# Optimization experiments

Measured on AMD Instinct MI355X. Metric: run time of the kernel, lower is better.

Reference implementation:

```python
import jax, jax.numpy as jnp
import numpy as np

L, H, C, V, BLK = 6, 16, 1024, 32000, 2048
B, T, TA = 2, 512, 512
DFF = 4 * C
STD = 0.02
PROJ_STD = 0.02 / np.sqrt(2 * L)  # c_proj init per module
SCALE = 1.0 / np.sqrt(C // H)


def setup_inputs() -> dict:
    key = jax.random.key(0)
    ks = iter(jax.random.split(key, 64))
    nrm = lambda shape, std=STD: jax.random.normal(next(ks), shape, jnp.float32) * std
    inp = {
        'idx': jax.random.randint(next(ks), (B, T), 0, V),
        'xa': jax.random.normal(next(ks), (B, TA, C), jnp.float32),
        'wte': nrm((V, C)),            # tied with lm_head
        'wpe': nrm((BLK, C)),
        'ln1_w': jnp.ones((L, C)), 'ln1_b': jnp.zeros((L, C)),
        'sa_wq': nrm((L, C, C)), 'sa_bq': jnp.zeros((L, C)),
        'sa_wk': nrm((L, C, C)), 'sa_bk': jnp.zeros((L, C)),
        'sa_wv': nrm((L, C, C)), 'sa_bv': jnp.zeros((L, C)),
        'sa_wo': nrm((L, C, C), PROJ_STD), 'sa_bo': jnp.zeros((L, C)),
        'ca_wq': nrm((L, C, C)), 'ca_bq': jnp.zeros((L, C)),
        'ca_wk': nrm((L, C, C)), 'ca_bk': jnp.zeros((L, C)),
        'ca_wv': nrm((L, C, C)), 'ca_bv': jnp.zeros((L, C)),
        'ca_wo': nrm((L, C, C), PROJ_STD), 'ca_bo': jnp.zeros((L, C)),
        'ln2_w': jnp.ones((L, C)), 'ln2_b': jnp.zeros((L, C)),
        'fc_w': nrm((L, C, DFF)), 'fc_b': jnp.zeros((L, DFF)),
        'pr_w': nrm((L, DFF, C), PROJ_STD), 'pr_b': jnp.zeros((L, C)),
        'lnf_w': jnp.ones((C,)), 'lnf_b': jnp.zeros((C,)),
    }
    return inp


def _ln(h, w, b):
    m = h.mean(-1, keepdims=True)
    v = jnp.mean((h - m) ** 2, -1, keepdims=True)
    return (h - m) * jax.lax.rsqrt(v + 1e-5) * w + b


def _gelu(h):  # new_gelu (tanh approximation)
    return 0.5 * h * (1.0 + jnp.tanh(np.sqrt(2.0 / np.pi) * (h + 0.044715 * h ** 3)))


def _attn(hq, hkv, wq, bq, wk, bk, wv, bv, wo, bo):
    # NB: the original applies a tril causal mask even for cross-attention.
    Bq, Tq, _ = hq.shape
    Tk = hkv.shape[1]
    D = C // H
    q = (hq @ wq + bq).reshape(Bq, Tq, H, D)
    k = (hkv @ wk + bk).reshape(Bq, Tk, H, D)
    v = (hkv @ wv + bv).reshape(Bq, Tk, H, D)
    att = jnp.einsum('bqhd,bkhd->bhqk', q, k) * SCALE
    mask = jnp.tril(jnp.ones((Tq, Tk), bool))
    att = jnp.where(mask, att, -jnp.inf)
    att = jax.nn.softmax(att, axis=-1)
    y = jnp.einsum('bhqk,bkhd->bqhd', att, v).reshape(Bq, Tq, C)
    return y @ wo + bo


def _forward(idx, xa, wte, wpe, ln1_w, ln1_b, sa_wq, sa_bq, sa_wk, sa_bk, sa_wv, sa_bv, sa_wo, sa_bo,
             ca_wq, ca_bq, ca_wk, ca_bk, ca_wv, ca_bv, ca_wo, ca_bo,
             ln2_w, ln2_b, fc_w, fc_b, pr_w, pr_b, lnf_w, lnf_b):
    t = idx.shape[1]
    x = wte[idx] + wpe[:t][None]  # [B,T,C]

    def block(h, p):
        (l1w, l1b, sqw, sqb, skw, skb, svw, svb, sow, sob,
         cqw, cqb, ckw, ckb, cvw, cvb, cow, cob,
         l2w, l2b, fw, fb, pw, pb) = p
        n = _ln(h, l1w, l1b)
        h = h + _attn(n, n, sqw, sqb, skw, skb, svw, svb, sow, sob)
        n = _ln(h, l1w, l1b)  # ln_1 reused for cross-attn, as in source
        h = h + _attn(n, xa, cqw, cqb, ckw, ckb, cvw, cvb, cow, cob)
        n = _ln(h, l2w, l2b)
        h = h + (_gelu(n @ fw + fb) @ pw + pb)
        return h, None

    xs = (ln1_w, ln1_b, sa_wq, sa_bq, sa_wk, sa_bk, sa_wv, sa_bv, sa_wo, sa_bo,
          ca_wq, ca_bq, ca_wk, ca_bk, ca_wv, ca_bv, ca_wo, ca_bo,
          ln2_w, ln2_b, fc_w, fc_b, pr_w, pr_b)
    x, _ = jax.lax.scan(block, x, xs)
    x = _ln(x, lnf_w, lnf_b)
    return x @ wte.T  # tied lm_head, [B,T,V]


def reference(idx, xa, wte, wpe, ln1_w, ln1_b, sa_wq, sa_bq, sa_wk, sa_bk, sa_wv, sa_bv, sa_wo, sa_bo,
              ca_wq, ca_bq, ca_wk, ca_bk, ca_wv, ca_bv, ca_wo, ca_bo,
              ln2_w, ln2_b, fc_w, fc_b, pr_w, pr_b, lnf_w, lnf_b):
    return _forward(idx, xa, wte, wpe, ln1_w, ln1_b, sa_wq, sa_bq, sa_wk, sa_bk, sa_wv, sa_bv, sa_wo, sa_bo,
                    ca_wq, ca_bq, ca_wk, ca_bk, ca_wv, ca_bv, ca_wo, ca_bo,
                    ln2_w, ln2_b, fc_w, fc_b, pr_w, pr_b, lnf_w, lnf_b)
```

## Files before the change

kernel.cpp:

```cpp
#include <hip/hip_runtime.h>
#include <math.h>

#define CC   1024
#define HH   16
#define DH   64
#define TT   512
#define NTOK 1024
#define DFF_ 4096
#define VV   32000
#define QKSCALE 0.125f

typedef unsigned short u16;
typedef __attribute__((ext_vector_type(8))) short short8;
typedef __attribute__((ext_vector_type(4))) float f32x4;

__device__ __forceinline__ u16 f2bf(float f) {
  union { float f; unsigned u; } v; v.f = f;
  unsigned r = v.u + 0x7FFFu + ((v.u >> 16) & 1u);
  return (u16)(r >> 16);
}
__device__ __forceinline__ float gelu_f(float h) {
  return 0.5f * h * (1.0f + tanhf(0.7978845608028654f * (h + 0.044715f * h * h * h)));
}

#define GLD16(gp, lp) __builtin_amdgcn_global_load_lds( \
    (const __attribute__((address_space(1))) void*)(gp), \
    (__attribute__((address_space(3))) void*)(lp), 16, 0, 0)

#define MFMA(a, b, c) __builtin_amdgcn_mfma_f32_16x16x32_bf16(a, b, c, 0, 0, 0)

__global__ __launch_bounds__(256) void embed_kernel(
    const int* __restrict__ idx, const float* __restrict__ wte,
    const float* __restrict__ wpe, float* __restrict__ x) {
  int row = blockIdx.x;
  int t = row & (TT - 1);
  int id = idx[row];
  const float4* a = (const float4*)(wte + (size_t)id * CC);
  const float4* p = (const float4*)(wpe + (size_t)t * CC);
  float4* o = (float4*)(x + (size_t)row * CC);
  int c = threadIdx.x;
  float4 va = a[c], vp = p[c];
  float4 ov;
  ov.x = va.x + vp.x; ov.y = va.y + vp.y; ov.z = va.z + vp.z; ov.w = va.w + vp.w;
  o[c] = ov;
}

__global__ __launch_bounds__(256) void ln_kernel(
    const float* __restrict__ x, const float* __restrict__ w,
    const float* __restrict__ b, u16* __restrict__ out) {
  int row = blockIdx.x, tid = threadIdx.x;
  float4 v = ((const float4*)(x + (size_t)row * CC))[tid];
  float s  = v.x + v.y + v.z + v.w;
  float sq = fmaf(v.x, v.x, fmaf(v.y, v.y, fmaf(v.z, v.z, v.w * v.w)));
  for (int o = 32; o > 0; o >>= 1) { s += __shfl_down(s, o); sq += __shfl_down(sq, o); }
  __shared__ float rs[4], rq[4];
  int wid = tid >> 6, lane = tid & 63;
  if (lane == 0) { rs[wid] = s; rq[wid] = sq; }
  __syncthreads();
  s  = rs[0] + rs[1] + rs[2] + rs[3];
  sq = rq[0] + rq[1] + rq[2] + rq[3];
  float mean = s * (1.0f / CC);
  float var  = sq * (1.0f / CC) - mean * mean;
  float rstd = 1.0f / sqrtf(var + 1e-5f);
  float4 wv = ((const float4*)w)[tid];
  float4 bv = ((const float4*)b)[tid];
  ushort4 o;
  o.x = f2bf((v.x - mean) * rstd * wv.x + bv.x);
  o.y = f2bf((v.y - mean) * rstd * wv.y + bv.y);
  o.z = f2bf((v.z - mean) * rstd * wv.z + bv.z);
  o.w = f2bf((v.w - mean) * rstd * wv.w + bv.w);
  ((ushort4*)(out + (size_t)row * CC))[tid] = o;
}

__global__ __launch_bounds__(256) void wtrans16_kernel(
    const float* __restrict__ w0, const float* __restrict__ w1,
    const float* __restrict__ w2, const float* __restrict__ w3,
    const float* __restrict__ w4, const float* __restrict__ w5,
    const float* __restrict__ w6, const float* __restrict__ w7,
    const float* __restrict__ fc, const float* __restrict__ pr,
    u16* __restrict__ wt) {
  const size_t M1 = 1048576;
  int z = blockIdx.z;
  const float* src;
  size_t doff;
  int sstr, dstr;
  if (z < 8) {
    src = z == 0 ? w0 : z == 1 ? w1 : z == 2 ? w2 : z == 3 ? w3
        : z == 4 ? w4 : z == 5 ? w5 : z == 6 ? w6 : w7;
    sstr = 1024; doff = (size_t)z * M1; dstr = 1024;
  } else if (z < 12) {
    int s = z - 8;
    src = fc + (size_t)s * 1024; sstr = 4096;
    doff = 8 * M1 + (size_t)s * M1; dstr = 1024;
  } else {
    int s = z - 12;
    src = pr + (size_t)s * M1; sstr = 1024;
    doff = 12 * M1 + (size_t)s * 1024; dstr = 4096;
  }
  __shared__ float t[32][33];
  int bx = blockIdx.x * 32, by = blockIdx.y * 32;
  int c = threadIdx.x & 31, r = threadIdx.x >> 5;
#pragma unroll
  for (int i = 0; i < 4; ++i)
    t[r + i * 8][c] = src[(size_t)(by + r + i * 8) * sstr + bx + c];
  __syncthreads();
#pragma unroll
  for (int i = 0; i < 4; ++i)
    wt[doff + (size_t)(bx + r + i * 8) * dstr + by + c] = f2bf(t[c][r + i * 8]);
}

__global__ __launch_bounds__(256) void convbf_kernel(
    const float* __restrict__ in, u16* __restrict__ out, int n4) {
  int i = blockIdx.x * 256 + threadIdx.x;
  if (i < n4) {
    float4 v = ((const float4*)in)[i];
    ushort4 o; o.x = f2bf(v.x); o.y = f2bf(v.y); o.z = f2bf(v.z); o.w = f2bf(v.w);
    ((ushort4*)out)[i] = o;
  }
}

template <int EPI, int MODE, int BM, int BN, int BK>
__global__ __launch_bounds__(256) void gemm_bf16_kernel(
    const u16* __restrict__ A, const u16* __restrict__ B,
    const float* __restrict__ bias, const float* __restrict__ bias2,
    const float* __restrict__ bias3, float* __restrict__ Cm,
    int K, int ldc, int whichbase) {
  constexpr int WM = BM / 2, WN = BN / 2, MF = WM / 16, NF = WN / 16;
  constexpr int KS = BK / 32;
  constexpr int NB = BK / 8;
  constexpr int PA = BM * BK / 2048;
  constexpr int PB = BN * BK / 2048;
  constexpr int RPP = 2048 / BK;
  __shared__ u16 As[2][BM * BK];
  __shared__ u16 Bs[2][BN * BK];
  int tid = threadIdx.x;
  int lane = tid & 63, wave = tid >> 6;
  int wr = wave >> 1, wc = wave & 1;
  int row0, col0;
  if (MODE == 2) {
    int id = blockIdx.x;
    int wg = (id & 7) * 250 + (id >> 3);
    row0 = (wg & 7) * BM;
    col0 = (wg >> 3) * BN;
  } else {
    row0 = blockIdx.y * BM;
    col0 = blockIdx.x * BN;
  }
  f32x4 acc[MF][NF];
#pragma unroll
  for (int m = 0; m < MF; ++m)
#pragma unroll
    for (int n = 0; n < NF; ++n) acc[m][n] = (f32x4){0.f, 0.f, 0.f, 0.f};

  int srow = tid / NB;
  int sblk = (BK == 64) ? ((tid & 7) ^ ((tid >> 3) & 7))
                        : ((tid & 3) ^ ((tid >> 3) & 3));
  const u16* Ab = A + (size_t)row0 * K;
  const u16* Bb = B + (size_t)col0 * K;
  int arow = wr * WM + (lane & 15);
  int brow = wc * WN + (lane & 15);
  int g8 = lane >> 4;

  auto stage = [&](int bufi, int k0) {
#pragma unroll
    for (int p = 0; p < PA; ++p)
      GLD16(Ab + (size_t)(p * RPP + srow) * K + k0 + sblk * 8,
            &As[bufi][p * 2048 + wave * 512]);
#pragma unroll
    for (int p = 0; p < PB; ++p)
      GLD16(Bb + (size_t)(p * RPP + srow) * K + k0 + sblk * 8,
            &Bs[bufi][p * 2048 + wave * 512]);
  };

  const int NT = K / BK;
  stage(0, 0);
  __syncthreads();
  for (int t = 0; t < NT; ++t) {
    int cur = t & 1;
    if (t + 1 < NT) stage(cur ^ 1, (t + 1) * BK);
    const u16* Ac = As[cur];
    const u16* Bc = Bs[cur];
#pragma unroll
    for (int ks = 0; ks < KS; ++ks) {
      short8 af[MF], bg[NF];
#pragma unroll
      for (int m = 0; m < MF; ++m) {
        int row = arow + m * 16;
        int off = (BK == 64) ? row * 64 + (((ks * 4 + g8) ^ (row & 7)) << 3)
                             : row * 32 + ((g8 ^ ((row >> 1) & 3)) << 3);
        af[m] = *(const short8*)&Ac[off];
      }
#pragma unroll
      for (int n = 0; n < NF; ++n) {
        int row = brow + n * 16;
        int off = (BK == 64) ? row * 64 + (((ks * 4 + g8) ^ (row & 7)) << 3)
                             : row * 32 + ((g8 ^ ((row >> 1) & 3)) << 3);
        bg[n] = *(const short8*)&Bc[off];
      }
      __builtin_amdgcn_s_setprio(1);
#pragma unroll
      for (int m = 0; m < MF; ++m)
#pragma unroll
        for (int n = 0; n < NF; ++n)
          acc[m][n] = MFMA(af[m], bg[n], acc[m][n]);
      __builtin_amdgcn_s_setprio(0);
    }
    __syncthreads();
  }

  int r0 = row0 + wr * WM + g8 * 4;
  int c0 = col0 + wc * WN + (lane & 15);

  if (EPI == 4) {
    u16* qb = (u16*)Cm;
#pragma unroll
    for (int m = 0; m < MF; ++m)
#pragma unroll
      for (int n = 0; n < NF; ++n) {
        int j = c0 + n * 16;
        int which = whichbase + (j >> 10);
        const float* bp = (j >> 10) == 0 ? bias : ((j >> 10) == 1 ? bias2 : bias3);
        float bj = bp ? bp[j & 1023] : 0.0f;
        int h = (j & 1023) >> 6, d = j & 63;
        int trow0 = r0 + m * 16;
        int b = trow0 >> 9, t0 = trow0 & 511;
        int bh = b * 16 + h;
        u16 vals[4];
#pragma unroll
        for (int r = 0; r < 4; ++r) vals[r] = f2bf(acc[m][n][r] + bj);
        if (which < 2) {
          u16* dst = qb + (size_t)which * 1048576 + (size_t)bh * 32768 + (size_t)t0 * 64 + d;
#pragma unroll
          for (int r = 0; r < 4; ++r) dst[(size_t)r * 64] = vals[r];
        } else {
          u16* dst = qb + 2 * 1048576 + (size_t)bh * 32768 + (size_t)d * 512 + t0;
          *(ushort4*)dst = *(ushort4*)vals;
        }
      }
    return;
  }

  float bj[NF];
#pragma unroll
  for (int n = 0; n < NF; ++n)
    bj[n] = bias ? bias[c0 + n * 16] : 0.0f;
  u16* Cb = (u16*)Cm;
#pragma unroll
  for (int m = 0; m < MF; ++m)
#pragma unroll
    for (int n = 0; n < NF; ++n)
#pragma unroll
      for (int r = 0; r < 4; ++r) {
        size_t off = (size_t)(r0 + m * 16 + r) * ldc + c0 + n * 16;
        float v = acc[m][n][r] + bj[n];
        if (EPI == 0) Cm[off] = v;
        else if (EPI == 1) Cm[off] += v;
        else if (EPI == 2) Cb[off] = f2bf(gelu_f(v));
      }
}

__global__ __launch_bounds__(256) void attn_kernel(
    const u16* __restrict__ qh, const u16* __restrict__ kh,
    const u16* __restrict__ vt, u16* __restrict__ y) {
  __shared__ u16 P[32 * 512];
  __shared__ float smax[4][32], ssum[4][32];
  int tid = threadIdx.x, lane = tid & 63, w = tid >> 6;
  int bx = blockIdx.x, bh = blockIdx.y;
  int q0 = bx * 32;
  int b = bh >> 4, h = bh & 15;
  const u16* qb = qh + (size_t)bh * 32768;
  const u16* kb = kh + (size_t)bh * 32768;
  const u16* vb = vt + (size_t)bh * 32768;
  int g = lane >> 4, c = lane & 15;

  short8 a[2][2];
#pragma unroll
  for (int rt = 0; rt < 2; ++rt)
#pragma unroll
    for (int ks = 0; ks < 2; ++ks)
      a[rt][ks] = *(const short8*)(qb + (size_t)(q0 + rt * 16 + c) * 64 + ks * 32 + g * 8);

  int lim = q0 + 31;
  int nct = (lim - w * 128) / 16 + 1;
  if (nct > 8) nct = 8;
  if (nct < 0) nct = 0;
  f32x4 s[2][8];
#pragma unroll
  for (int rt = 0; rt < 2; ++rt)
#pragma unroll
    for (int ct = 0; ct < 8; ++ct) s[rt][ct] = (f32x4){0.f, 0.f, 0.f, 0.f};
  for (int ct = 0; ct < nct; ++ct) {
    int n0 = w * 128 + ct * 16;
#pragma unroll
    for (int ks = 0; ks < 2; ++ks) {
      short8 bf = *(const short8*)(kb + (size_t)(n0 + c) * 64 + ks * 32 + g * 8);
      s[0][ct] = MFMA(a[0][ks], bf, s[0][ct]);
      s[1][ct] = MFMA(a[1][ks], bf, s[1][ct]);
    }
  }

  float mx[2][4];
#pragma unroll
  for (int rt = 0; rt < 2; ++rt)
#pragma unroll
    for (int r = 0; r < 4; ++r) mx[rt][r] = -1e30f;
  for (int ct = 0; ct < nct; ++ct) {
    int col = w * 128 + ct * 16 + c;
#pragma unroll
    for (int rt = 0; rt < 2; ++rt)
#pragma unroll
      for (int r = 0; r < 4; ++r) {
        int trow = q0 + rt * 16 + g * 4 + r;
        float v = s[rt][ct][r] * QKSCALE;
        if (col > trow) v = -1e30f;
        s[rt][ct][r] = v;
        mx[rt][r] = fmaxf(mx[rt][r], v);
      }
  }
#pragma unroll
  for (int off = 1; off < 16; off <<= 1)
#pragma unroll
    for (int rt = 0; rt < 2; ++rt)
#pragma unroll
      for (int r = 0; r < 4; ++r) mx[rt][r] = fmaxf(mx[rt][r], __shfl_xor(mx[rt][r], off));
  if (c == 0)
#pragma unroll
    for (int rt = 0; rt < 2; ++rt)
#pragma unroll
      for (int r = 0; r < 4; ++r) smax[w][rt * 16 + g * 4 + r] = mx[rt][r];
  __syncthreads();

  float m_[2][4], sum[2][4];
#pragma unroll
  for (int rt = 0; rt < 2; ++rt)
#pragma unroll
    for (int r = 0; r < 4; ++r) {
      int row = rt * 16 + g * 4 + r;
      m_[rt][r] = fmaxf(fmaxf(smax[0][row], smax[1][row]), fmaxf(smax[2][row], smax[3][row]));
      sum[rt][r] = 0.f;
    }
  for (int ct = 0; ct < nct; ++ct) {
    int col = w * 128 + ct * 16 + c;
    int blk = col >> 3, cl = col & 7;
#pragma unroll
    for (int rt = 0; rt < 2; ++rt)
#pragma unroll
      for (int r = 0; r < 4; ++r) {
        float p = __expf(s[rt][ct][r] - m_[rt][r]);
        sum[rt][r] += p;
        int row = rt * 16 + g * 4 + r;
        int hsh = (row ^ (row >> 2)) & 7;
        P[row * 512 + ((blk ^ hsh) << 3) + cl] = f2bf(p);
      }
  }
#pragma unroll
  for (int off = 1; off < 16; off <<= 1)
#pragma unroll
    for (int rt = 0; rt < 2; ++rt)
#pragma unroll
      for (int r = 0; r < 4; ++r) sum[rt][r] += __shfl_xor(sum[rt][r], off);
  if (c == 0)
#pragma unroll
    for (int rt = 0; rt < 2; ++rt)
#pragma unroll
      for (int r = 0; r < 4; ++r) ssum[w][rt * 16 + g * 4 + r] = sum[rt][r];
  __syncthreads();

  float li[2][4];
#pragma unroll
  for (int rt = 0; rt < 2; ++rt)
#pragma unroll
    for (int r = 0; r < 4; ++r) {
      int row = rt * 16 + g * 4 + r;
      li[rt][r] = 1.0f / (ssum[0][row] + ssum[1][row] + ssum[2][row] + ssum[3][row]);
    }

  int rt2 = w >> 1, nh = w & 1;
  f32x4 o[2];
  o[0] = (f32x4){0.f, 0.f, 0.f, 0.f};
  o[1] = (f32x4){0.f, 0.f, 0.f, 0.f};
  int nks = bx + 1;
  int prow = rt2 * 16 + c;
  int phsh = (prow ^ (prow >> 2)) & 7;
  for (int ks = 0; ks < nks; ++ks) {
    short8 pa = *(const short8*)&P[prow * 512 + (((ks * 4 + g) ^ phsh) << 3)];
#pragma unroll
    for (int nt = 0; nt < 2; ++nt) {
      int d = nh * 32 + nt * 16 + c;
      short8 vf = *(const short8*)(vb + (size_t)d * 512 + ks * 32 + g * 8);
      o[nt] = MFMA(pa, vf, o[nt]);
    }
  }
#pragma unroll
  for (int nt = 0; nt < 2; ++nt)
#pragma unroll
    for (int r = 0; r < 4; ++r) {
      int trow = q0 + rt2 * 16 + g * 4 + r;
      float val = o[nt][r] * li[rt2][r];
      y[(size_t)(b * 512 + trow) * 1024 + h * 64 + nh * 32 + nt * 16 + c] = f2bf(val);
    }
}

extern "C" void kernel_launch(void* const* d_in, const int* in_sizes, int n_in,
                              void* d_out, int out_size, void* d_ws, size_t ws_size,
                              hipStream_t stream) {
  const int*   idx   = (const int*)d_in[0];
  const float* xa    = (const float*)d_in[1];
  const float* wte   = (const float*)d_in[2];
  const float* wpe   = (const float*)d_in[3];
  const float* ln1_w = (const float*)d_in[4];
  const float* ln1_b = (const float*)d_in[5];
  const float* sa_wq = (const float*)d_in[6];
  const float* sa_bq = (const float*)d_in[7];
  const float* sa_wk = (const float*)d_in[8];
  const float* sa_bk = (const float*)d_in[9];
  const float* sa_wv = (const float*)d_in[10];
  const float* sa_bv = (const float*)d_in[11];
  const float* sa_wo = (const float*)d_in[12];
  const float* sa_bo = (const float*)d_in[13];
  const float* ca_wq = (const float*)d_in[14];
  const float* ca_bq = (const float*)d_in[15];
  const float* ca_wk = (const float*)d_in[16];
  const float* ca_bk = (const float*)d_in[17];
  const float* ca_wv = (const float*)d_in[18];
  const float* ca_bv = (const float*)d_in[19];
  const float* ca_wo = (const float*)d_in[20];
  const float* ca_bo = (const float*)d_in[21];
  const float* ln2_w = (const float*)d_in[22];
  const float* ln2_b = (const float*)d_in[23];
  const float* fc_w  = (const float*)d_in[24];
  const float* fc_b  = (const float*)d_in[25];
  const float* pr_w  = (const float*)d_in[26];
  const float* pr_b  = (const float*)d_in[27];
  const float* lnf_w = (const float*)d_in[28];
  const float* lnf_b = (const float*)d_in[29];

  const size_t M1 = 1048576;
  float* ws     = (float*)d_ws;
  float* x      = ws;
  u16* qkvh  = (u16*)(x + M1);
  u16* nbf   = qkvh + 3 * M1;
  u16* ybf   = nbf + M1;
  u16* hmbf  = ybf + M1;
  u16* xabf  = hmbf + 4 * M1;
  u16* wtebf = xabf + M1;
  u16* wT    = wtebf + (size_t)VV * CC;

  const size_t oQKV = 0, oWO = 3 * M1, oCQ = 4 * M1, oCKV = 5 * M1,
               oCWO = 7 * M1, oFC = 8 * M1, oPR = 12 * M1;

  embed_kernel<<<NTOK, 256, 0, stream>>>(idx, wte, wpe, x);
  convbf_kernel<<<(VV * CC / 4 + 255) / 256, 256, 0, stream>>>(wte, wtebf, VV * CC / 4);
  convbf_kernel<<<(NTOK * CC / 4 + 255) / 256, 256, 0, stream>>>(xa, xabf, NTOK * CC / 4);

  for (int l = 0; l < 6; ++l) {
    size_t wofs = (size_t)l * CC * CC;
    size_t bofs = (size_t)l * CC;
    size_t mofs = (size_t)l * CC * DFF_;

    wtrans16_kernel<<<dim3(32, 32, 16), 256, 0, stream>>>(
        sa_wq + wofs, sa_wk + wofs, sa_wv + wofs, sa_wo + wofs,
        ca_wq + wofs, ca_wk + wofs, ca_wv + wofs, ca_wo + wofs,
        fc_w + mofs, pr_w + mofs, wT);

    ln_kernel<<<NTOK, 256, 0, stream>>>(x, ln1_w + bofs, ln1_b + bofs, nbf);
    gemm_bf16_kernel<4, 0, 64, 128, 64><<<dim3(24, 16), 256, 0, stream>>>(
        nbf, wT + oQKV, sa_bq + bofs, sa_bk + bofs, sa_bv + bofs,
        (float*)qkvh, CC, 0, 0);
    attn_kernel<<<dim3(16, 32), 256, 0, stream>>>(qkvh, qkvh + M1, qkvh + 2 * M1, ybf);
    gemm_bf16_kernel<1, 0, 64, 64, 64><<<dim3(16, 16), 256, 0, stream>>>(
        ybf, wT + oWO, sa_bo + bofs, nullptr, nullptr, x, CC, CC, 0);

    ln_kernel<<<NTOK, 256, 0, stream>>>(x, ln1_w + bofs, ln1_b + bofs, nbf);
    gemm_bf16_kernel<4, 0, 64, 64, 64><<<dim3(16, 16), 256, 0, stream>>>(
        nbf, wT + oCQ, ca_bq + bofs, nullptr, nullptr, (float*)qkvh, CC, 0, 0);
    gemm_bf16_kernel<4, 0, 64, 128, 64><<<dim3(16, 16), 256, 0, stream>>>(
        xabf, wT + oCKV, ca_bk + bofs, ca_bv + bofs, nullptr,
        (float*)qkvh, CC, 0, 1);
    attn_kernel<<<dim3(16, 32), 256, 0, stream>>>(qkvh, qkvh + M1, qkvh + 2 * M1, ybf);
    gemm_bf16_kernel<1, 0, 64, 64, 64><<<dim3(16, 16), 256, 0, stream>>>(
        ybf, wT + oCWO, ca_bo + bofs, nullptr, nullptr, x, CC, CC, 0);

    ln_kernel<<<NTOK, 256, 0, stream>>>(x, ln2_w + bofs, ln2_b + bofs, nbf);
    gemm_bf16_kernel<2, 0, 128, 128, 32><<<dim3(32, 8), 256, 0, stream>>>(
        nbf, wT + oFC, fc_b + (size_t)l * DFF_, nullptr, nullptr,
        (float*)hmbf, CC, DFF_, 0);
    gemm_bf16_kernel<1, 0, 64, 64, 64><<<dim3(16, 16), 256, 0, stream>>>(
        hmbf, wT + oPR, pr_b + bofs, nullptr, nullptr, x, DFF_, CC, 0);
  }

  ln_kernel<<<NTOK, 256, 0, stream>>>(x, lnf_w, lnf_b, nbf);
  gemm_bf16_kernel<0, 2, 128, 128, 32><<<dim3(2000), 256, 0, stream>>>(
      nbf, wtebf, nullptr, nullptr, nullptr, (float*)d_out, CC, VV, 0);
}
```

Measured before the change: 1.670 ms.

## Fuse wte bf16 conversion into lm_head GEMM, batch weight transposes, merge cross-attn QKV

The lm_head GEMM now reads fp32 wte directly and converts it to bf16 in registers while staging into LDS. This removes the separate full-vocab conversion pass and its 64MB bf16 copy. All six layers' weight transposes run in one launch when the workspace is large enough, and cross-attention Q and KV projections are merged into a single MODE-3 launch. Several GEMM tile shapes are also changed (smaller BM for the output projections, BK=64 for FC). The lm_head B load is now synchronous register staging instead of async global-to-LDS, which may expose more latency.

```diff
diff --git a/kernel.cpp b/kernel.cpp
--- a/kernel.cpp
+++ b/kernel.cpp
@@ -72,30 +72,34 @@
   ((ushort4*)(out + (size_t)row * CC))[tid] = o;
 }
 
-__global__ __launch_bounds__(256) void wtrans16_kernel(
+__global__ __launch_bounds__(256) void wtransL_kernel(
     const float* __restrict__ w0, const float* __restrict__ w1,
     const float* __restrict__ w2, const float* __restrict__ w3,
     const float* __restrict__ w4, const float* __restrict__ w5,
     const float* __restrict__ w6, const float* __restrict__ w7,
     const float* __restrict__ fc, const float* __restrict__ pr,
-    u16* __restrict__ wt) {
+    u16* __restrict__ wt, size_t dls, int lbase) {
   const size_t M1 = 1048576;
   int z = blockIdx.z;
+  int l = lbase + (z >> 4), slot = z & 15;
+  size_t wofs = (size_t)l * M1;
+  size_t mofs = (size_t)l * 4 * M1;
   const float* src;
-  size_t doff;
+  size_t doff = (size_t)(l - lbase) * dls;
   int sstr, dstr;
-  if (z < 8) {
-    src = z == 0 ? w0 : z == 1 ? w1 : z == 2 ? w2 : z == 3 ? w3
-        : z == 4 ? w4 : z == 5 ? w5 : z == 6 ? w6 : w7;
-    sstr = 1024; doff = (size_t)z * M1; dstr = 1024;
-  } else if (z < 12) {
-    int s = z - 8;
-    src = fc + (size_t)s * 1024; sstr = 4096;
-    doff = 8 * M1 + (size_t)s * M1; dstr = 1024;
+  if (slot < 8) {
+    const float* base = slot == 0 ? w0 : slot == 1 ? w1 : slot == 2 ? w2
+                      : slot == 3 ? w3 : slot == 4 ? w4 : slot == 5 ? w5
+                      : slot == 6 ? w6 : w7;
+    src = base + wofs; sstr = 1024; doff += (size_t)slot * M1; dstr = 1024;
+  } else if (slot < 12) {
+    int s = slot - 8;
+    src = fc + mofs + (size_t)s * 1024; sstr = 4096;
+    doff += 8 * M1 + (size_t)s * M1; dstr = 1024;
   } else {
-    int s = z - 12;
-    src = pr + (size_t)s * M1; sstr = 1024;
-    doff = 12 * M1 + (size_t)s * 1024; dstr = 4096;
+    int s = slot - 12;
+    src = pr + mofs + (size_t)s * M1; sstr = 1024;
+    doff += 12 * M1 + (size_t)s * 1024; dstr = 4096;
   }
   __shared__ float t[32][33];
   int bx = blockIdx.x * 32, by = blockIdx.y * 32;
@@ -121,7 +125,8 @@
 
 template <int EPI, int MODE, int BM, int BN, int BK>
 __global__ __launch_bounds__(256) void gemm_bf16_kernel(
-    const u16* __restrict__ A, const u16* __restrict__ B,
+    const u16* __restrict__ A, const u16* __restrict__ A2,
+    const u16* __restrict__ B, const u16* __restrict__ B2,
     const float* __restrict__ bias, const float* __restrict__ bias2,
     const float* __restrict__ bias3, float* __restrict__ Cm,
     int K, int ldc, int whichbase) {
@@ -137,11 +142,21 @@
   int lane = tid & 63, wave = tid >> 6;
   int wr = wave >> 1, wc = wave & 1;
   int row0, col0;
+  bool isq = true;
+  const u16* Ause = A;
+  const u16* Buse = B;
   if (MODE == 2) {
     int id = blockIdx.x;
     int wg = (id & 7) * 250 + (id >> 3);
     row0 = (wg & 7) * BM;
     col0 = (wg >> 3) * BN;
+  } else if (MODE == 3) {
+    int bx = blockIdx.x;
+    isq = bx < (1024 / BN);
+    Ause = isq ? A : A2;
+    Buse = isq ? B : B2;
+    col0 = (isq ? bx : bx - 1024 / BN) * BN;
+    row0 = blockIdx.y * BM;
   } else {
     row0 = blockIdx.y * BM;
     col0 = blockIdx.x * BN;
@@ -155,31 +170,13 @@
   int srow = tid / NB;
   int sblk = (BK == 64) ? ((tid & 7) ^ ((tid >> 3) & 7))
                         : ((tid & 3) ^ ((tid >> 3) & 3));
-  const u16* Ab = A + (size_t)row0 * K;
-  const u16* Bb = B + (size_t)col0 * K;
+  const u16* Ab = Ause + (size_t)row0 * K;
   int arow = wr * WM + (lane & 15);
   int brow = wc * WN + (lane & 15);
   int g8 = lane >> 4;
-
-  auto stage = [&](int bufi, int k0) {
-#pragma unroll
-    for (int p = 0; p < PA; ++p)
-      GLD16(Ab + (size_t)(p * RPP + srow) * K + k0 + sblk * 8,
-            &As[bufi][p * 2048 + wave * 512]);
-#pragma unroll
-    for (int p = 0; p < PB; ++p)
-      GLD16(Bb + (size_t)(p * RPP + srow) * K + k0 + sblk * 8,
-            &Bs[bufi][p * 2048 + wave * 512]);
-  };
-
   const int NT = K / BK;
-  stage(0, 0);
-  __syncthreads();
-  for (int t = 0; t < NT; ++t) {
-    int cur = t & 1;
-    if (t + 1 < NT) stage(cur ^ 1, (t + 1) * BK);
-    const u16* Ac = As[cur];
-    const u16* Bc = Bs[cur];
+
+  auto compute = [&](const u16* Ac, const u16* Bc) {
 #pragma unroll
     for (int ks = 0; ks < KS; ++ks) {
       short8 af[MF], bg[NF];
@@ -205,7 +202,65 @@
           acc[m][n] = MFMA(af[m], bg[n], acc[m][n]);
       __builtin_amdgcn_s_setprio(0);
     }
+  };
+
+  if constexpr (MODE == 2) {
+    const float* Bf = (const float*)B;
+    int bsr = tid >> 2;
+    int bkb = tid & 3;
+    float4 rb0, rb1, rb2, rb3;
+    auto loadB = [&](int k0) {
+      const float* p0 = Bf + (size_t)(col0 + bsr) * 1024 + k0 + bkb * 8;
+      const float* p1 = Bf + (size_t)(col0 + 64 + bsr) * 1024 + k0 + bkb * 8;
+      rb0 = *(const float4*)p0; rb1 = *(const float4*)(p0 + 4);
+      rb2 = *(const float4*)p1; rb3 = *(const float4*)(p1 + 4);
+    };
+    auto writeB = [&](int bufi) {
+      u16 t0[8] = {f2bf(rb0.x), f2bf(rb0.y), f2bf(rb0.z), f2bf(rb0.w),
+                   f2bf(rb1.x), f2bf(rb1.y), f2bf(rb1.z), f2bf(rb1.w)};
+      u16 t1[8] = {f2bf(rb2.x), f2bf(rb2.y), f2bf(rb2.z), f2bf(rb2.w),
+                   f2bf(rb3.x), f2bf(rb3.y), f2bf(rb3.z), f2bf(rb3.w)};
+      int r1 = 64 + bsr;
+      *(short8*)&Bs[bufi][bsr * 32 + ((bkb ^ ((bsr >> 1) & 3)) << 3)] = *(short8*)t0;
+      *(short8*)&Bs[bufi][r1 * 32 + ((bkb ^ ((r1 >> 1) & 3)) << 3)] = *(short8*)t1;
+    };
+    auto stageA = [&](int bufi, int k0) {
+#pragma unroll
+      for (int p = 0; p < PA; ++p)
+        GLD16(Ab + (size_t)(p * RPP + srow) * K + k0 + sblk * 8,
+              &As[bufi][p * 2048 + wave * 512]);
+    };
+    loadB(0);
+    stageA(0, 0);
+    writeB(0);
     __syncthreads();
+    for (int t = 0; t < NT; ++t) {
+      int cur = t & 1;
+      if (t + 1 < NT) { loadB((t + 1) * BK); stageA(cur ^ 1, (t + 1) * BK); }
+      compute(As[cur], Bs[cur]);
+      if (t + 1 < NT) writeB(cur ^ 1);
+      __syncthreads();
+    }
+  } else {
+    const u16* Bb = Buse + (size_t)col0 * K;
+    auto stage = [&](int bufi, int k0) {
+#pragma unroll
+      for (int p = 0; p < PA; ++p)
+        GLD16(Ab + (size_t)(p * RPP + srow) * K + k0 + sblk * 8,
+              &As[bufi][p * 2048 + wave * 512]);
+#pragma unroll
+      for (int p = 0; p < PB; ++p)
+        GLD16(Bb + (size_t)(p * RPP + srow) * K + k0 + sblk * 8,
+              &Bs[bufi][p * 2048 + wave * 512]);
+    };
+    stage(0, 0);
+    __syncthreads();
+    for (int t = 0; t < NT; ++t) {
+      int cur = t & 1;
+      if (t + 1 < NT) stage(cur ^ 1, (t + 1) * BK);
+      compute(As[cur], Bs[cur]);
+      __syncthreads();
+    }
   }
 
   int r0 = row0 + wr * WM + g8 * 4;
@@ -218,8 +273,8 @@
 #pragma unroll
       for (int n = 0; n < NF; ++n) {
         int j = c0 + n * 16;
-        int which = whichbase + (j >> 10);
-        const float* bp = (j >> 10) == 0 ? bias : ((j >> 10) == 1 ? bias2 : bias3);
+        int which = (MODE == 3 ? (isq ? 0 : 1) : whichbase) + (j >> 10);
+        const float* bp = which == 0 ? bias : (which == 1 ? bias2 : bias3);
         float bj = bp ? bp[j & 1023] : 0.0f;
         int h = (j & 1023) >> 6, d = j & 63;
         int trow0 = r0 + m * 16;
@@ -443,53 +498,59 @@
   u16* ybf   = nbf + M1;
   u16* hmbf  = ybf + M1;
   u16* xabf  = hmbf + 4 * M1;
-  u16* wtebf = xabf + M1;
-  u16* wT    = wtebf + (size_t)VV * CC;
+  u16* wT    = xabf + M1;
+
+  const bool full = ws_size >= 226492416ull;
+  const size_t wls = full ? 16 * M1 : 0;
 
   const size_t oQKV = 0, oWO = 3 * M1, oCQ = 4 * M1, oCKV = 5 * M1,
                oCWO = 7 * M1, oFC = 8 * M1, oPR = 12 * M1;
 
   embed_kernel<<<NTOK, 256, 0, stream>>>(idx, wte, wpe, x);
-  convbf_kernel<<<(VV * CC / 4 + 255) / 256, 256, 0, stream>>>(wte, wtebf, VV * CC / 4);
   convbf_kernel<<<(NTOK * CC / 4 + 255) / 256, 256, 0, stream>>>(xa, xabf, NTOK * CC / 4);
+  if (full)
+    wtransL_kernel<<<dim3(32, 32, 96), 256, 0, stream>>>(
+        sa_wq, sa_wk, sa_wv, sa_wo, ca_wq, ca_wk, ca_wv, ca_wo,
+        fc_w, pr_w, wT, wls, 0);
 
   for (int l = 0; l < 6; ++l) {
-    size_t wofs = (size_t)l * CC * CC;
     size_t bofs = (size_t)l * CC;
-    size_t mofs = (size_t)l * CC * DFF_;
-
-    wtrans16_kernel<<<dim3(32, 32, 16), 256, 0, stream>>>(
-        sa_wq + wofs, sa_wk + wofs, sa_wv + wofs, sa_wo + wofs,
-        ca_wq + wofs, ca_wk + wofs, ca_wv + wofs, ca_wo + wofs,
-        fc_w + mofs, pr_w + mofs, wT);
+    u16* wTl = wT + (size_t)l * wls;
+
+    if (!full)
+      wtransL_kernel<<<dim3(32, 32, 16), 256, 0, stream>>>(
+          sa_wq, sa_wk, sa_wv, sa_wo, ca_wq, ca_wk, ca_wv, ca_wo,
+          fc_w, pr_w, wT, 0, l);
 
     ln_kernel<<<NTOK, 256, 0, stream>>>(x, ln1_w + bofs, ln1_b + bofs, nbf);
     gemm_bf16_kernel<4, 0, 64, 128, 64><<<dim3(24, 16), 256, 0, stream>>>(
-        nbf, wT + oQKV, sa_bq + bofs, sa_bk + bofs, sa_bv + bofs,
-        (float*)qkvh, CC, 0, 0);
+        nbf, nullptr, wTl + oQKV, nullptr, sa_bq + bofs, sa_bk + bofs,
+        sa_bv + bofs, (float*)qkvh, CC, 0, 0);
     attn_kernel<<<dim3(16, 32), 256, 0, stream>>>(qkvh, qkvh + M1, qkvh + 2 * M1, ybf);
-    gemm_bf16_kernel<1, 0, 64, 64, 64><<<dim3(16, 16), 256, 0, stream>>>(
-        ybf, wT + oWO, sa_bo + bofs, nullptr, nullptr, x, CC, CC, 0);
+    gemm_bf16_kernel<1, 0, 32, 64, 64><<<dim3(16, 32), 256, 0, stream>>>(
+        ybf, nullptr, wTl + oWO, nullptr, sa_bo + bofs, nullptr, nullptr,
+        x, CC, CC, 0);
 
     ln_kernel<<<NTOK, 256, 0, stream>>>(x, ln1_w + bofs, ln1_b + bofs, nbf);
-    gemm_bf16_kernel<4, 0, 64, 64, 64><<<dim3(16, 16), 256, 0, stream>>>(
-        nbf, wT + oCQ, ca_bq + bofs, nullptr, nullptr, (float*)qkvh, CC, 0, 0);
-    gemm_bf16_kernel<4, 0, 64, 128, 64><<<dim3(16, 16), 256, 0, stream>>>(
-        xabf, wT + oCKV, ca_bk + bofs, ca_bv + bofs, nullptr,
-        (float*)qkvh, CC, 0, 1);
+    gemm_bf16_kernel<4, 3, 64, 64, 64><<<dim3(48, 16), 256, 0, stream>>>(
+        nbf, xabf, wTl + oCQ, wTl + oCKV, ca_bq + bofs, ca_bk + bofs,
+        ca_bv + bofs, (float*)qkvh, CC, 0, 0);
     attn_kernel<<<dim3(16, 32), 256, 0, stream>>>(qkvh, qkvh + M1, qkvh + 2 * M1, ybf);
-    gemm_bf16_kernel<1, 0, 64, 64, 64><<<dim3(16, 16), 256, 0, stream>>>(
-        ybf, wT + oCWO, ca_bo + bofs, nullptr, nullptr, x, CC, CC, 0);
+    gemm_bf16_kernel<1, 0, 32, 64, 64><<<dim3(16, 32), 256, 0, stream>>>(
+        ybf, nullptr, wTl + oCWO, nullptr, ca_bo + bofs, nullptr, nullptr,
+        x, CC, CC, 0);
 
     ln_kernel<<<NTOK, 256, 0, stream>>>(x, ln2_w + bofs, ln2_b + bofs, nbf);
-    gemm_bf16_kernel<2, 0, 128, 128, 32><<<dim3(32, 8), 256, 0, stream>>>(
-        nbf, wT + oFC, fc_b + (size_t)l * DFF_, nullptr, nullptr,
-        (float*)hmbf, CC, DFF_, 0);
-    gemm_bf16_kernel<1, 0, 64, 64, 64><<<dim3(16, 16), 256, 0, stream>>>(
-        hmbf, wT + oPR, pr_b + bofs, nullptr, nullptr, x, DFF_, CC, 0);
+    gemm_bf16_kernel<2, 0, 64, 128, 64><<<dim3(32, 16), 256, 0, stream>>>(
+        nbf, nullptr, wTl + oFC, nullptr, fc_b + (size_t)l * DFF_, nullptr,
+        nullptr, (float*)hmbf, CC, DFF_, 0);
+    gemm_bf16_kernel<1, 0, 32, 64, 64><<<dim3(16, 32), 256, 0, stream>>>(
+        hmbf, nullptr, wTl + oPR, nullptr, pr_b + bofs, nullptr, nullptr,
+        x, DFF_, CC, 0);
   }
 
   ln_kernel<<<NTOK, 256, 0, stream>>>(x, lnf_w, lnf_b, nbf);
   gemm_bf16_kernel<0, 2, 128, 128, 32><<<dim3(2000), 256, 0, stream>>>(
-      nbf, wtebf, nullptr, nullptr, nullptr, (float*)d_out, CC, VV, 0);
-}
+      nbf, nullptr, (const u16*)wte, nullptr, nullptr, nullptr, nullptr,
+      (float*)d_out, CC, VV, 0);
+}
```

Measured after the change: 1.649 ms. Within noise of the previous version (-1.2%).
